# Kernel optimization log

Measured on AMD Instinct MI355X. Metric: run time of the kernel, lower is better.

## Reference

```python
import jax, jax.numpy as jnp
import numpy as np

DIM = 256
HEADS = 8
HD = DIM // HEADS          # 32
WS = 8                     # window size
TOPK = 4
SCALE = HD ** -0.5


def setup_inputs() -> dict:
    key = jax.random.key(0)
    k1, k2, k3 = jax.random.split(key, 3)
    B, H, W = 8, 64, 64
    x = jax.random.normal(k1, (B, DIM, H, W), dtype=jnp.float32)
    # 1x1 conv weights (BN folded -> weight + bias), fan-in scaled to keep logits sane
    w_qkv = jax.random.normal(k2, (3 * DIM, DIM), dtype=jnp.float32) / np.sqrt(DIM)
    b_qkv = jnp.zeros((3 * DIM,), dtype=jnp.float32)
    w_proj = jax.random.normal(k3, (DIM, DIM), dtype=jnp.float32) / np.sqrt(DIM)
    b_proj = jnp.zeros((DIM,), dtype=jnp.float32)
    return {"x": x, "w_qkv": w_qkv, "b_qkv": b_qkv, "w_proj": w_proj, "b_proj": b_proj}


def _window_partition(t, ws):
    # t: [BH, D, H, W] -> [BH, R, ws*ws, D]
    bh, d, h, w = t.shape
    gh, gw = h // ws, w // ws
    t = t.reshape(bh, d, gh, ws, gw, ws)
    t = t.transpose(0, 2, 4, 3, 5, 1)          # [BH, gh, gw, ws, ws, D]
    return t.reshape(bh, gh * gw, ws * ws, d)


def reference(x, w_qkv, b_qkv, w_proj, b_proj):
    B, C, H, W = x.shape
    gh, gw = H // WS, W // WS
    R, T = gh * gw, WS * WS
    BH = B * HEADS

    # qkv 1x1 conv
    qkv = jnp.einsum('bchw,oc->bohw', x, w_qkv) + b_qkv[None, :, None, None]
    q, k, v = jnp.split(qkv, 3, axis=1)                       # each [B, C, H, W]

    def to_bh(t):
        return t.reshape(BH, HD, H, W)

    q_w = _window_partition(to_bh(q), WS)                     # [BH, R, T, HD]
    k_w = _window_partition(to_bh(k), WS)
    v_w = _window_partition(to_bh(v), WS)

    # region-level routing: mean-pooled region tokens
    q_r = q_w.mean(axis=2)                                    # [BH, R, HD]
    k_r = k_w.mean(axis=2)
    attn_r = jnp.einsum('brd,bkd->brk', q_r, k_r) * SCALE     # [BH, R, R]
    topk = min(TOPK, R)
    _, topk_idx = jax.lax.top_k(attn_r, topk)                 # [BH, R, K]

    # gather top-k key/value windows per query region
    bidx = jnp.arange(BH)[:, None, None]
    k_sel = k_w[bidx, topk_idx]                               # [BH, R, K, T, HD]
    v_sel = v_w[bidx, topk_idx]
    k_sel = k_sel.reshape(BH, R, topk * T, HD)
    v_sel = v_sel.reshape(BH, R, topk * T, HD)

    # token-level attention inside routed regions
    attn = jnp.einsum('brtd,brsd->brts', q_w, k_sel) * SCALE  # [BH, R, T, K*T]
    attn = jax.nn.softmax(attn, axis=-1)
    out_w = jnp.einsum('brts,brsd->brtd', attn, v_sel)        # [BH, R, T, HD]

    # window reverse -> [BH, HD, H, W]
    out = out_w.reshape(BH, gh, gw, WS, WS, HD)
    out = out.transpose(0, 5, 1, 3, 2, 4).reshape(BH, HD, H, W)
    out = out.reshape(B, C, H, W)

    out = jnp.einsum('bchw,oc->bohw', out, w_proj) + b_proj[None, :, None, None]
    return out
```

## Files before the change

### kernel.cpp

```cpp
#include <hip/hip_runtime.h>
#include <hip/hip_bf16.h>

#define ATT_SCALE 0.17677669529663687f
#define EXP_C1 0.2550349235534668f
#define EXP_C2 23.083120654223400f

typedef short v8s __attribute__((ext_vector_type(8)));
typedef float v4f __attribute__((ext_vector_type(4)));
typedef float v16f __attribute__((ext_vector_type(16)));
typedef const __attribute__((address_space(1))) unsigned int gu32;
typedef __attribute__((address_space(3))) unsigned int lu32;

__device__ __forceinline__ void g2l16(const void* g, void* l) {
  __builtin_amdgcn_global_load_lds((gu32*)g, (lu32*)l, 16, 0, 0);
}

__device__ __forceinline__ float bflo(unsigned u){ union{unsigned i;float f;}x; x.i=u<<16; return x.f; }
__device__ __forceinline__ float bfhi(unsigned u){ union{unsigned i;float f;}x; x.i=u&0xffff0000u; return x.f; }
__device__ __forceinline__ unsigned short bf16r(float v){
  __hip_bfloat16 h = __float2bfloat16(v);
  return *reinterpret_cast<unsigned short*>(&h);
}
__device__ __forceinline__ unsigned pack_bf2(float a, float b){
  return (unsigned)bf16r(a) | ((unsigned)bf16r(b) << 16);
}
__device__ __forceinline__ unsigned cvtpk(float lo, float hi){
  unsigned r;
  asm("v_cvt_pk_bf16_f32 %0, %1, %2" : "=v"(r) : "v"(lo), "v"(hi));
  return r;
}
__device__ __forceinline__ void pl32swap(unsigned &a, unsigned &b){
  asm volatile("v_permlane32_swap_b32 %0, %1" : "+v"(a), "+v"(b));
}

__global__ __launch_bounds__(256) void k_wprep(const float* __restrict__ w_qkv,
                                               const float* __restrict__ w_proj,
                                               unsigned short* __restrict__ Wq,
                                               unsigned short* __restrict__ Wp) {
  const int m = blockIdx.x, t = threadIdx.x;
  const float* src = (m < 768) ? (w_qkv + m*256) : (w_proj + (size_t)(m - 768)*256);
  unsigned short* dst = (m < 768) ? (Wq + m*256) : (Wp + (size_t)(m - 768)*256);
  int col = (t & ~63) | ((t & 63) ^ ((m & 7) << 3));
  dst[col] = bf16r(src[t]);
}

__global__ __launch_bounds__(256) void k_fqkv(
    const float* __restrict__ x,
    const unsigned short* __restrict__ Wq,
    const float* __restrict__ bias,
    unsigned short* __restrict__ qbuf, unsigned short* __restrict__ kbuf,
    unsigned short* __restrict__ vbuf, float* __restrict__ part) {
  __shared__ __align__(16) char lds[65536];
  const int tid = threadIdx.x;
  const int wv = tid >> 6, lane = tid & 63;
  const int nt = blockIdx.x;
  const int b = nt >> 6, pc = nt & 63;
  const int p0 = pc << 6;
  float* pbuf = (float*)(lds + 32768);

  #pragma unroll
  for (int cc = 0; cc < 4; ++cc) {
    float hi[16];
    const float* xp = x + ((size_t)(b*256 + cc*64 + wv*16))*4096 + p0 + lane;
    #pragma unroll
    for (int i = 0; i < 16; ++i) hi[i] = xp[(size_t)i*4096];

    #pragma unroll
    for (int i = 0; i < 16; ++i) {
      float s = hi[i];
      s += __shfl_xor(s, 1);
      s += __shfl_xor(s, 2);
      s += __shfl_xor(s, 4);
      if ((lane & 7) == 0) pbuf[cc*512 + (wv*16 + i)*8 + (lane >> 3)] = s;
    }
    #pragma unroll
    for (int gi = 0; gi < 2; ++gi) {
      uint4 uh;
      uh.x = pack_bf2(hi[gi*8+0], hi[gi*8+1]); uh.y = pack_bf2(hi[gi*8+2], hi[gi*8+3]);
      uh.z = pack_bf2(hi[gi*8+4], hi[gi*8+5]); uh.w = pack_bf2(hi[gi*8+6], hi[gi*8+7]);
      int off = lane*512 + cc*128 + ((wv*32 + gi*16) ^ ((lane & 7) << 4));
      *(uint4*)(lds + off) = uh;
    }
  }
  __syncthreads();
  {
    const size_t pbase = (size_t)(b*64 + pc)*2048;
    #pragma unroll
    for (int s = 0; s < 8; ++s) part[pbase + s*256 + tid] = pbuf[s*256 + tid];
  }
  __syncthreads();

  const char* wlanebase = (const char*)Wq + ((size_t)(lane >> 3))*512 + (lane & 7)*16;

  {
    #pragma unroll
    for (int o = 0; o < 4; ++o) {
      int op = wv*4 + o;
      g2l16(wlanebase + (size_t)(op*8)*512, lds + 32768 + op*1024);
    }
    asm volatile("s_waitcnt vmcnt(0)" ::: "memory");
    __syncthreads();
  }

  #pragma unroll
  for (int m = 0; m < 6; ++m) {
    v4f acc[2][4];
    #pragma unroll
    for (int i = 0; i < 2; ++i)
      #pragma unroll
      for (int j = 0; j < 4; ++j) acc[i][j] = (v4f){0.f,0.f,0.f,0.f};

    #pragma unroll
    for (int kt = 0; kt < 4; ++kt) {
      const int s = m*4 + kt;
      const int cur = s & 1;
      if (s < 23) {
        const int s2 = s + 1;
        const int m2 = s2 >> 2, kt2 = s2 & 3;
        char* dst = lds + 32768 + (cur^1)*16384;
        #pragma unroll
        for (int o = 0; o < 4; ++o) {
          int op = wv*4 + o;
          g2l16(wlanebase + (size_t)(m2*128 + op*8)*512 + kt2*128, dst + op*1024);
        }
      }
      const char* wb = lds + 32768 + cur*16384;
      #pragma unroll
      for (int kk = 0; kk < 2; ++kk) {
        const int kb = kk*64 + ((lane>>4)<<4);
        v8s a[2], bfr[4];
        #pragma unroll
        for (int i = 0; i < 2; ++i) {
          int mr = wv*32 + i*16 + (lane & 15);
          a[i] = *(const v8s*)(wb + mr*128 + (kb ^ ((mr & 7) << 4)));
        }
        #pragma unroll
        for (int j = 0; j < 4; ++j) {
          int nr = j*16 + (lane & 15);
          bfr[j] = *(const v8s*)(lds + nr*512 + kt*128 + (kb ^ ((nr & 7) << 4)));
        }
        #pragma unroll
        for (int i = 0; i < 2; ++i)
          #pragma unroll
          for (int j = 0; j < 4; ++j)
            acc[i][j] = __builtin_amdgcn_mfma_f32_16x16x32_bf16(a[i], bfr[j], acc[i][j], 0, 0, 0);
      }
      if (s < 23) {
        asm volatile("s_waitcnt vmcnt(0)" ::: "memory");
        __syncthreads();
      }
    }

    if (m < 4) {
      unsigned short* outbuf = (m < 2) ? qbuf : kbuf;
      #pragma unroll
      for (int i = 0; i < 2; ++i) {
        int o = m*128 + wv*32 + i*16 + ((lane >> 4) << 2);
        int head = (o >> 5) & 7, d0 = o & 31;
        float b0 = bias[o], b1 = bias[o+1], b2 = bias[o+2], b3 = bias[o+3];
        #pragma unroll
        for (int j = 0; j < 4; ++j) {
          int p = nt*64 + j*16 + (lane & 15);
          int bb = p >> 12, ploc = p & 4095;
          int h = ploc >> 6, w = ploc & 63;
          int rr = ((h >> 3) << 3) | (w >> 3), tt = ((h & 7) << 3) | (w & 7);
          int bh = bb*8 + head;
          uint2 u;
          u.x = pack_bf2(acc[i][j][0] + b0, acc[i][j][1] + b1);
          u.y = pack_bf2(acc[i][j][2] + b2, acc[i][j][3] + b3);
          *(uint2*)(outbuf + (size_t)(((bh << 6) | rr)*64 + tt)*32 + d0) = u;
        }
      }
    } else {
      #pragma unroll
      for (int i = 0; i < 2; ++i) {
        int o = m*128 + wv*32 + i*16 + ((lane >> 4) << 2);
        int vch = o - 512;
        int head = vch >> 5, d0 = vch & 31;
        float bv[4] = {bias[o], bias[o+1], bias[o+2], bias[o+3]};
        #pragma unroll
        for (int j = 0; j < 4; ++j) {
          int p = nt*64 + j*16 + (lane & 15);
          int bb = p >> 12, ploc = p & 4095;
          int h = ploc >> 6, w = ploc & 63;
          int rr = ((h >> 3) << 3) | (w >> 3), tt = ((h & 7) << 3) | (w & 7);
          int bh = bb*8 + head;
          size_t base = ((size_t)((bh << 6) | rr)*32 + d0)*64 + tt;
          #pragma unroll
          for (int c = 0; c < 4; ++c)
            vbuf[base + (size_t)c*64] = bf16r(acc[i][j][c] + bv[c]);
        }
      }
    }
  }
}

__global__ __launch_bounds__(256) void k_xmr(const float* __restrict__ part,
                                             float* __restrict__ xmean) {
  const int blk = blockIdx.x;
  const int item = blk & 7;
  const int b = blk >> 6, rh = (blk >> 3) & 7;
  const int t = threadIdx.x;
  const int flat = item*256 + t;
  float acc = 0.f;
  const float* pp = part + (size_t)(b*64 + rh*8)*2048 + flat;
  #pragma unroll
  for (int j = 0; j < 8; ++j) acc += pp[(size_t)j*2048];
  const int c = flat >> 3, wc = flat & 7;
  xmean[(size_t)((b*256 + c) << 6) + (rh << 3) + wc] = acc * 0.015625f;
}

__global__ __launch_bounds__(256) void k_route(const float* __restrict__ xmean,
                                               const float* __restrict__ w_qkv,
                                               const float* __restrict__ b_qkv,
                                               int* __restrict__ topk) {
  __shared__ float xm[128][64];
  __shared__ float qr[64][33];
  __shared__ float kr[64][33];
  const int bh = blockIdx.x, b = bh >> 3, head = bh & 7;
  const int tid = threadIdx.x;
  const int d = tid & 31, r0 = tid >> 5;
  float qacc[8], kacc[8];
  const float bq = b_qkv[head*32 + d], bk = b_qkv[256 + head*32 + d];
  #pragma unroll
  for (int i = 0; i < 8; ++i) { qacc[i] = bq; kacc[i] = bk; }

  for (int c0 = 0; c0 < 256; c0 += 128) {
    __syncthreads();
    #pragma unroll
    for (int i = 0; i < 32; ++i) {
      int idx = i*256 + tid;
      int row = idx >> 6, col = idx & 63;
      xm[row][col] = xmean[(size_t)(b*256 + c0 + row)*64 + col];
    }
    __syncthreads();
    const float* wqp = w_qkv + (head*32 + d)*256 + c0;
    const float* wkp = w_qkv + (256 + head*32 + d)*256 + c0;
    for (int c = 0; c < 128; ++c) {
      float wq = wqp[c], wk = wkp[c];
      #pragma unroll
      for (int i = 0; i < 8; ++i) {
        float xv = xm[c][r0 + 8*i];
        qacc[i] += wq * xv;
        kacc[i] += wk * xv;
      }
    }
  }
  #pragma unroll
  for (int i = 0; i < 8; ++i) { qr[r0+8*i][d] = qacc[i]; kr[r0+8*i][d] = kacc[i]; }
  __syncthreads();

  float* ar = &xm[0][0];
  for (int item = tid; item < 4096; item += 256) {
    int i = item >> 6, j = item & 63;
    float s = 0.f;
    #pragma unroll
    for (int dd = 0; dd < 32; ++dd) s += qr[i][dd]*kr[j][dd];
    ar[i*64 + j] = s;
  }
  __syncthreads();
  if (tid < 64) {
    for (int kk = 0; kk < 4; ++kk) {
      float best = -3e38f; int bj = 0;
      for (int j = 0; j < 64; ++j) {
        float v = ar[tid*64 + j];
        if (v > best) { best = v; bj = j; }
      }
      ar[tid*64 + bj] = -3e38f;
      topk[(bh*64 + tid)*4 + kk] = bj;
    }
  }
}

__global__ __launch_bounds__(256) void k_proj(
    const unsigned short* __restrict__ Wp,
    const unsigned short* __restrict__ Bmat,
    const float* __restrict__ bias,
    float* __restrict__ outp) {
  __shared__ __align__(16) char lds[81920];
  const int tid = threadIdx.x;
  const int wv = tid >> 6, lane = tid & 63;
  const int nt = blockIdx.x;

  v4f acc[4][4];
  #pragma unroll
  for (int i = 0; i < 4; ++i)
    #pragma unroll
    for (int j = 0; j < 4; ++j) acc[i][j] = (v4f){0.f,0.f,0.f,0.f};

  const char* wlanebase = (const char*)Wp + ((size_t)(lane>>3))*512 + (lane&7)*16;
  const size_t prowlane = (size_t)(nt*64 + (lane>>3))*512 + (lane&7)*16;

  {
    #pragma unroll
    for (int o = 0; o < 8; ++o) {
      int op = wv*8 + o;
      g2l16(wlanebase + (size_t)(op*8)*512, lds + op*1024);
    }
    #pragma unroll
    for (int o = 0; o < 2; ++o) {
      int op = wv*2 + o;
      g2l16((const char*)Bmat + prowlane + (size_t)(op*8)*512, lds + 65536 + op*1024);
    }
    asm volatile("s_waitcnt vmcnt(0)" ::: "memory");
    __syncthreads();
  }

  #pragma unroll
  for (int kt = 0; kt < 4; ++kt) {
    const int cur = kt & 1;
    if (kt < 3) {
      const int k0b = (kt + 1)*128;
      char* wb = lds + (cur^1)*32768;
      char* xb = lds + 65536 + (cur^1)*8192;
      #pragma unroll
      for (int o = 0; o < 8; ++o) {
        int op = wv*8 + o;
        g2l16(wlanebase + (size_t)(op*8)*512 + k0b, wb + op*1024);
      }
      #pragma unroll
      for (int o = 0; o < 2; ++o) {
        int op = wv*2 + o;
        g2l16((const char*)Bmat + prowlane + (size_t)(op*8)*512 + k0b, xb + op*1024);
      }
    }
    const char* wb = lds + cur*32768;
    const char* xb = lds + 65536 + cur*8192;
    #pragma unroll
    for (int kk = 0; kk < 2; ++kk) {
      const int kb = kk*64 + ((lane>>4)<<4);
      v8s a[4], b[4];
      #pragma unroll
      for (int i = 0; i < 4; ++i) {
        int mr = wv*64 + i*16 + (lane & 15);
        a[i] = *(const v8s*)(wb + mr*128 + (kb ^ ((mr & 7) << 4)));
      }
      #pragma unroll
      for (int j = 0; j < 4; ++j) {
        int nr = j*16 + (lane & 15);
        b[j] = *(const v8s*)(xb + nr*128 + (kb ^ ((nr & 7) << 4)));
      }
      #pragma unroll
      for (int i = 0; i < 4; ++i)
        #pragma unroll
        for (int j = 0; j < 4; ++j)
          acc[i][j] = __builtin_amdgcn_mfma_f32_16x16x32_bf16(a[i], b[j], acc[i][j], 0, 0, 0);
    }
    if (kt < 3) {
      asm volatile("s_waitcnt vmcnt(0)" ::: "memory");
      __syncthreads();
    }
  }

  #pragma unroll
  for (int i = 0; i < 4; ++i) {
    int o = wv*64 + i*16 + ((lane >> 4) << 2);
    float b0 = bias[o], b1 = bias[o+1], b2 = bias[o+2], b3 = bias[o+3];
    #pragma unroll
    for (int j = 0; j < 4; ++j) {
      int p = nt*64 + j*16 + (lane & 15);
      int bb = p >> 12, ploc = p & 4095;
      float* dst = outp + ((size_t)(bb*256 + o))*4096 + ploc;
      dst[0]     = acc[i][j][0] + b0;
      dst[4096]  = acc[i][j][1] + b1;
      dst[8192]  = acc[i][j][2] + b2;
      dst[12288] = acc[i][j][3] + b3;
    }
  }
}

__global__ __launch_bounds__(256) void k_attn(const unsigned short* __restrict__ qw,
                                              const unsigned short* __restrict__ kw,
                                              const unsigned short* __restrict__ vwt,
                                              const int* __restrict__ topk,
                                              unsigned short* __restrict__ owt) {
  const int lane = threadIdx.x & 63;
  const int W = blockIdx.x*4 + (threadIdx.x >> 6);
  const int bh = W >> 6, rr = W & 63;
  const int lo5 = lane & 31, hi = lane >> 5;
  const int b = bh >> 3, head = bh & 7;

  const unsigned short* qb = qw + (size_t)(bh*64 + rr)*2048;
  v8s qf[2][2];
  #pragma unroll
  for (int qt = 0; qt < 2; ++qt)
    #pragma unroll
    for (int ck = 0; ck < 2; ++ck)
      qf[qt][ck] = *(const v8s*)(qb + (qt*32 + lo5)*32 + ck*16 + hi*8);

  int idx4[4];
  #pragma unroll
  for (int w = 0; w < 4; ++w) idx4[w] = topk[(bh*64 + rr)*4 + w];

  v16f O[2];
  #pragma unroll
  for (int qt = 0; qt < 2; ++qt)
    #pragma unroll
    for (int r = 0; r < 16; ++r) O[qt][r] = 0.f;
  float lsum[2] = {0.f, 0.f};

  #pragma unroll
  for (int w = 0; w < 4; ++w) {
    const unsigned short* kb = kw  + (size_t)(bh*64 + idx4[w])*2048;
    const unsigned short* vb = vwt + (size_t)(bh*64 + idx4[w])*2048;
    v8s kf[2][2], vf[4];
    #pragma unroll
    for (int kt = 0; kt < 2; ++kt)
      #pragma unroll
      for (int ck = 0; ck < 2; ++ck)
        kf[kt][ck] = *(const v8s*)(kb + (kt*32 + lo5)*32 + ck*16 + hi*8);
    #pragma unroll
    for (int mk = 0; mk < 4; ++mk)
      vf[mk] = *(const v8s*)(vb + lo5*64 + mk*16 + hi*8);

    v16f S[2][2];
    #pragma unroll
    for (int kt = 0; kt < 2; ++kt)
      #pragma unroll
      for (int qt = 0; qt < 2; ++qt) {
        v16f z;
        #pragma unroll
        for (int r = 0; r < 16; ++r) z[r] = 0.f;
        z = __builtin_amdgcn_mfma_f32_32x32x16_bf16(kf[kt][0], qf[qt][0], z, 0, 0, 0);
        S[kt][qt] = __builtin_amdgcn_mfma_f32_32x32x16_bf16(kf[kt][1], qf[qt][1], z, 0, 0, 0);
      }

    #pragma unroll
    for (int kt = 0; kt < 2; ++kt) {
      #pragma unroll
      for (int qt = 0; qt < 2; ++qt) {
        float p[16];
        #pragma unroll
        for (int r = 0; r < 16; ++r)
          p[r] = __builtin_amdgcn_exp2f(__builtin_fmaf(S[kt][qt][r], EXP_C1, -EXP_C2));
        float s01 = (p[0]+p[1]) + (p[2]+p[3]);
        float s23 = (p[4]+p[5]) + (p[6]+p[7]);
        float s45 = (p[8]+p[9]) + (p[10]+p[11]);
        float s67 = (p[12]+p[13]) + (p[14]+p[15]);
        lsum[qt] += (s01 + s23) + (s45 + s67);

        unsigned wh[8], wl[8];
        #pragma unroll
        for (int i = 0; i < 8; ++i) {
          wh[i] = cvtpk(p[2*i], p[2*i+1]);
          float l0 = p[2*i]   - bflo(wh[i]);
          float l1 = p[2*i+1] - bfhi(wh[i]);
          wl[i] = cvtpk(l0, l1);
        }
        pl32swap(wh[0], wh[2]); pl32swap(wh[1], wh[3]);
        pl32swap(wh[4], wh[6]); pl32swap(wh[5], wh[7]);
        pl32swap(wl[0], wl[2]); pl32swap(wl[1], wl[3]);
        pl32swap(wl[4], wl[6]); pl32swap(wl[5], wl[7]);
        union { unsigned u[4]; v8s v; } fA, fB;
        fA.u[0] = wh[0]; fA.u[1] = wh[1]; fA.u[2] = wh[2]; fA.u[3] = wh[3];
        fB.u[0] = wl[0]; fB.u[1] = wl[1]; fB.u[2] = wl[2]; fB.u[3] = wl[3];
        O[qt] = __builtin_amdgcn_mfma_f32_32x32x16_bf16(fA.v, vf[2*kt], O[qt], 0, 0, 0);
        O[qt] = __builtin_amdgcn_mfma_f32_32x32x16_bf16(fB.v, vf[2*kt], O[qt], 0, 0, 0);
        fA.u[0] = wh[4]; fA.u[1] = wh[5]; fA.u[2] = wh[6]; fA.u[3] = wh[7];
        fB.u[0] = wl[4]; fB.u[1] = wl[5]; fB.u[2] = wl[6]; fB.u[3] = wl[7];
        O[qt] = __builtin_amdgcn_mfma_f32_32x32x16_bf16(fA.v, vf[2*kt+1], O[qt], 0, 0, 0);
        O[qt] = __builtin_amdgcn_mfma_f32_32x32x16_bf16(fB.v, vf[2*kt+1], O[qt], 0, 0, 0);
      }
    }
  }

  float linv[2];
  #pragma unroll
  for (int qt = 0; qt < 2; ++qt) {
    float t = lsum[qt] + __shfl_xor(lsum[qt], 32);
    linv[qt] = 1.0f / t;
  }

  #pragma unroll
  for (int qt = 0; qt < 2; ++qt) {
    #pragma unroll
    for (int r = 0; r < 16; ++r) {
      int q = (r & 3) + 8*(r >> 2) + 4*hi;
      float li = __shfl(linv[qt], q);
      float val = O[qt][r] * li;
      int tok = qt*32 + q;
      int h = ((rr >> 3) << 3) | (tok >> 3);
      int wcol = ((rr & 7) << 3) | (tok & 7);
      int pg = (b << 12) | (h << 6) | wcol;
      int col = ((head >> 1) << 6) | ((((head & 1) << 5) + lo5) ^ ((tok & 7) << 3));
      owt[(size_t)pg*256 + col] = bf16r(val);
    }
  }
}

extern "C" void kernel_launch(void* const* d_in, const int* in_sizes, int n_in,
                              void* d_out, int out_size, void* d_ws, size_t ws_size,
                              hipStream_t stream) {
  (void)in_sizes; (void)n_in; (void)out_size; (void)ws_size;
  const float* x      = (const float*)d_in[0];
  const float* w_qkv  = (const float*)d_in[1];
  const float* b_qkv  = (const float*)d_in[2];
  const float* w_proj = (const float*)d_in[3];
  const float* b_proj = (const float*)d_in[4];
  float* out = (float*)d_out;

  char* ws = (char*)d_ws;
  unsigned short* owt = (unsigned short*)ws;
  unsigned short* Wq  = (unsigned short*)(ws + 16777216);
  unsigned short* Wp  = (unsigned short*)(ws + 17170432);
  unsigned short* qw  = (unsigned short*)(ws + 17301504);
  unsigned short* kw  = (unsigned short*)(ws + 34078720);
  unsigned short* vwt = (unsigned short*)(ws + 50855936);
  float* part         = (float*)(ws + 67633152);
  float* xmean        = (float*)(ws + 71827456);
  int* topk           = (int*)(ws + 72351744);

  k_wprep<<<dim3(1024), 256, 0, stream>>>(w_qkv, w_proj, Wq, Wp);
  k_fqkv <<<dim3(512),  256, 0, stream>>>(x, Wq, b_qkv, qw, kw, vwt, part);
  k_xmr  <<<dim3(512),  256, 0, stream>>>(part, xmean);
  k_route<<<dim3(64),   256, 0, stream>>>(xmean, w_qkv, b_qkv, topk);
  k_attn <<<dim3(1024), 256, 0, stream>>>(qw, kw, vwt, topk, owt);
  k_proj <<<dim3(512),  256, 0, stream>>>(Wp, owt, b_proj, out);
}
```

Before: 119.9 us.

## Overlap QKV epilogue stores with next tile's MFMA via double accumulators; add setprio

```diff
diff --git a/kernel.cpp b/kernel.cpp
--- a/kernel.cpp
+++ b/kernel.cpp
@@ -92,70 +92,22 @@
 
   const char* wlanebase = (const char*)Wq + ((size_t)(lane >> 3))*512 + (lane & 7)*16;
 
-  {
+  auto stage = [&](int s2, int buf) {
+    const int m2 = s2 >> 2, kt2 = s2 & 3;
+    char* dst = lds + 32768 + buf*16384;
     #pragma unroll
     for (int o = 0; o < 4; ++o) {
       int op = wv*4 + o;
-      g2l16(wlanebase + (size_t)(op*8)*512, lds + 32768 + op*1024);
-    }
-    asm volatile("s_waitcnt vmcnt(0)" ::: "memory");
-    __syncthreads();
-  }
-
-  #pragma unroll
-  for (int m = 0; m < 6; ++m) {
-    v4f acc[2][4];
-    #pragma unroll
-    for (int i = 0; i < 2; ++i)
-      #pragma unroll
-      for (int j = 0; j < 4; ++j) acc[i][j] = (v4f){0.f,0.f,0.f,0.f};
-
-    #pragma unroll
-    for (int kt = 0; kt < 4; ++kt) {
-      const int s = m*4 + kt;
-      const int cur = s & 1;
-      if (s < 23) {
-        const int s2 = s + 1;
-        const int m2 = s2 >> 2, kt2 = s2 & 3;
-        char* dst = lds + 32768 + (cur^1)*16384;
-        #pragma unroll
-        for (int o = 0; o < 4; ++o) {
-          int op = wv*4 + o;
-          g2l16(wlanebase + (size_t)(m2*128 + op*8)*512 + kt2*128, dst + op*1024);
-        }
-      }
-      const char* wb = lds + 32768 + cur*16384;
-      #pragma unroll
-      for (int kk = 0; kk < 2; ++kk) {
-        const int kb = kk*64 + ((lane>>4)<<4);
-        v8s a[2], bfr[4];
-        #pragma unroll
-        for (int i = 0; i < 2; ++i) {
-          int mr = wv*32 + i*16 + (lane & 15);
-          a[i] = *(const v8s*)(wb + mr*128 + (kb ^ ((mr & 7) << 4)));
-        }
-        #pragma unroll
-        for (int j = 0; j < 4; ++j) {
-          int nr = j*16 + (lane & 15);
-          bfr[j] = *(const v8s*)(lds + nr*512 + kt*128 + (kb ^ ((nr & 7) << 4)));
-        }
-        #pragma unroll
-        for (int i = 0; i < 2; ++i)
-          #pragma unroll
-          for (int j = 0; j < 4; ++j)
-            acc[i][j] = __builtin_amdgcn_mfma_f32_16x16x32_bf16(a[i], bfr[j], acc[i][j], 0, 0, 0);
-      }
-      if (s < 23) {
-        asm volatile("s_waitcnt vmcnt(0)" ::: "memory");
-        __syncthreads();
-      }
-    }
-
-    if (m < 4) {
-      unsigned short* outbuf = (m < 2) ? qbuf : kbuf;
+      g2l16(wlanebase + (size_t)(m2*128 + op*8)*512 + kt2*128, dst + op*1024);
+    }
+  };
+
+  auto epilogue = [&](int mm, v4f (*acc)[4]) {
+    if (mm < 4) {
+      unsigned short* outbuf = (mm < 2) ? qbuf : kbuf;
       #pragma unroll
       for (int i = 0; i < 2; ++i) {
-        int o = m*128 + wv*32 + i*16 + ((lane >> 4) << 2);
+        int o = mm*128 + wv*32 + i*16 + ((lane >> 4) << 2);
         int head = (o >> 5) & 7, d0 = o & 31;
         float b0 = bias[o], b1 = bias[o+1], b2 = bias[o+2], b3 = bias[o+3];
         #pragma unroll
@@ -174,7 +126,7 @@
     } else {
       #pragma unroll
       for (int i = 0; i < 2; ++i) {
-        int o = m*128 + wv*32 + i*16 + ((lane >> 4) << 2);
+        int o = mm*128 + wv*32 + i*16 + ((lane >> 4) << 2);
         int vch = o - 512;
         int head = vch >> 5, d0 = vch & 31;
         float bv[4] = {bias[o], bias[o+1], bias[o+2], bias[o+3]};
@@ -192,7 +144,63 @@
         }
       }
     }
-  }
+  };
+
+  v4f accA[2][4], accB[2][4];
+
+  stage(0, 0);
+  asm volatile("s_waitcnt vmcnt(0)" ::: "memory");
+  __syncthreads();
+
+  #pragma unroll
+  for (int s = 0; s < 24; ++s) {
+    const int m = s >> 2, kt = s & 3, cur = s & 1;
+    v4f (*acc)[4] = (m & 1) ? accB : accA;
+    if (kt == 0) {
+      #pragma unroll
+      for (int i = 0; i < 2; ++i)
+        #pragma unroll
+        for (int j = 0; j < 4; ++j) acc[i][j] = (v4f){0.f,0.f,0.f,0.f};
+    }
+    if (s < 23) stage(s + 1, cur ^ 1);
+    if (kt == 0 && m > 0) {
+      __builtin_amdgcn_sched_barrier(0);
+      epilogue(m - 1, (m & 1) ? accA : accB);
+      __builtin_amdgcn_sched_barrier(0);
+    }
+    {
+      const char* wb = lds + 32768 + cur*16384;
+      __builtin_amdgcn_s_setprio(1);
+      #pragma unroll
+      for (int kk = 0; kk < 2; ++kk) {
+        const int kb = kk*64 + ((lane>>4)<<4);
+        v8s a[2], bfr[4];
+        #pragma unroll
+        for (int i = 0; i < 2; ++i) {
+          int mr = wv*32 + i*16 + (lane & 15);
+          a[i] = *(const v8s*)(wb + mr*128 + (kb ^ ((mr & 7) << 4)));
+        }
+        #pragma unroll
+        for (int j = 0; j < 4; ++j) {
+          int nr = j*16 + (lane & 15);
+          bfr[j] = *(const v8s*)(lds + nr*512 + kt*128 + (kb ^ ((nr & 7) << 4)));
+        }
+        #pragma unroll
+        for (int i = 0; i < 2; ++i)
+          #pragma unroll
+          for (int j = 0; j < 4; ++j)
+            acc[i][j] = __builtin_amdgcn_mfma_f32_16x16x32_bf16(a[i], bfr[j], acc[i][j], 0, 0, 0);
+      }
+      __builtin_amdgcn_s_setprio(0);
+    }
+    if (s < 23) {
+      if (kt == 0 && m == 5)      asm volatile("s_waitcnt vmcnt(32)" ::: "memory");
+      else if (kt == 0 && m > 0)  asm volatile("s_waitcnt vmcnt(8)"  ::: "memory");
+      else                        asm volatile("s_waitcnt vmcnt(0)"  ::: "memory");
+      __syncthreads();
+    }
+  }
+  epilogue(5, accB);
 }
 
 __global__ __launch_bounds__(256) void k_xmr(const float* __restrict__ part,
@@ -326,6 +334,7 @@
     }
     const char* wb = lds + cur*32768;
     const char* xb = lds + 65536 + cur*8192;
+    __builtin_amdgcn_s_setprio(1);
     #pragma unroll
     for (int kk = 0; kk < 2; ++kk) {
       const int kb = kk*64 + ((lane>>4)<<4);
@@ -346,6 +355,7 @@
         for (int j = 0; j < 4; ++j)
           acc[i][j] = __builtin_amdgcn_mfma_f32_16x16x32_bf16(a[i], b[j], acc[i][j], 0, 0, 0);
     }
+    __builtin_amdgcn_s_setprio(0);
     if (kt < 3) {
       asm volatile("s_waitcnt vmcnt(0)" ::: "memory");
       __syncthreads();
@@ -414,6 +424,7 @@
       vf[mk] = *(const v8s*)(vb + lo5*64 + mk*16 + hi*8);
 
     v16f S[2][2];
+    __builtin_amdgcn_s_setprio(1);
     #pragma unroll
     for (int kt = 0; kt < 2; ++kt)
       #pragma unroll
@@ -424,6 +435,7 @@
         z = __builtin_amdgcn_mfma_f32_32x32x16_bf16(kf[kt][0], qf[qt][0], z, 0, 0, 0);
         S[kt][qt] = __builtin_amdgcn_mfma_f32_32x32x16_bf16(kf[kt][1], qf[qt][1], z, 0, 0, 0);
       }
+    __builtin_amdgcn_s_setprio(0);
 
     #pragma unroll
     for (int kt = 0; kt < 2; ++kt) {
@@ -454,12 +466,16 @@
         union { unsigned u[4]; v8s v; } fA, fB;
         fA.u[0] = wh[0]; fA.u[1] = wh[1]; fA.u[2] = wh[2]; fA.u[3] = wh[3];
         fB.u[0] = wl[0]; fB.u[1] = wl[1]; fB.u[2] = wl[2]; fB.u[3] = wl[3];
+        __builtin_amdgcn_s_setprio(1);
         O[qt] = __builtin_amdgcn_mfma_f32_32x32x16_bf16(fA.v, vf[2*kt], O[qt], 0, 0, 0);
         O[qt] = __builtin_amdgcn_mfma_f32_32x32x16_bf16(fB.v, vf[2*kt], O[qt], 0, 0, 0);
+        __builtin_amdgcn_s_setprio(0);
         fA.u[0] = wh[4]; fA.u[1] = wh[5]; fA.u[2] = wh[6]; fA.u[3] = wh[7];
         fB.u[0] = wl[4]; fB.u[1] = wl[5]; fB.u[2] = wl[6]; fB.u[3] = wl[7];
+        __builtin_amdgcn_s_setprio(1);
         O[qt] = __builtin_amdgcn_mfma_f32_32x32x16_bf16(fA.v, vf[2*kt+1], O[qt], 0, 0, 0);
         O[qt] = __builtin_amdgcn_mfma_f32_32x32x16_bf16(fB.v, vf[2*kt+1], O[qt], 0, 0, 0);
+        __builtin_amdgcn_s_setprio(0);
       }
     }
   }
```

New measurement: 117.4 us. -2.1%, faster.
